# Kernel tuning notes

Measured on AMD Instinct MI355X. Metric: run time of the kernel, lower is better.

The kernel has to match this reference:

```python
import jax, jax.numpy as jnp
import numpy as np

D_HID = 512
N_HEADS = 16
D_HEAD = D_HID // N_HEADS  # 32
D_FFN = 2048
B, N = 4, 1024
FACTOR = 0.5 / np.sqrt(D_HEAD)
EPS = 1e-5


def layer_norm(x, g, b):
    m = x.mean(-1, keepdims=True)
    v = ((x - m) ** 2).mean(-1, keepdims=True)
    return (x - m) / jnp.sqrt(v + EPS) * g + b


def setup_inputs() -> dict:
    key = jax.random.key(0)
    ks = jax.random.split(key, 24)
    s = 0.02
    p = lambda k, shape: jax.random.normal(k, shape, jnp.float32) * s
    inp = {
        'H': jax.random.normal(ks[0], (B, N, D_HID), jnp.float32),
        'V': jax.random.normal(ks[1], (B, N, 3, D_HID), jnp.float32),
        'D_batch': jax.random.normal(ks[2], (B, N, N), jnp.float32),
        'rbf_bias': jax.random.normal(ks[3], (B, 1, N, N), jnp.float32),
        'H_mask': jax.random.randint(ks[4], (B, N), 0, 2, jnp.int32),
        # attention sublayer params
        'g1': jnp.ones((D_HID,), jnp.float32), 'beta1': jnp.zeros((D_HID,), jnp.float32),
        'Wq': p(ks[5], (D_HID, 4 * D_HID)), 'bq': p(ks[6], (4 * D_HID,)),
        'Wk': p(ks[7], (D_HID, 4 * D_HID)), 'bk': p(ks[8], (4 * D_HID,)),
        'Wv': p(ks[9], (D_HID, D_HID)), 'bv': p(ks[10], (D_HID,)),
        'Wvv': p(ks[11], (D_HID, D_HID)),
        'Wo': p(ks[12], (D_HID, D_HID)), 'bo': p(ks[13], (D_HID,)),
        'Wvo': p(ks[14], (D_HID, D_HID)),
        # GVP FFN sublayer params
        'g2': jnp.ones((D_HID,), jnp.float32), 'beta2': jnp.zeros((D_HID,), jnp.float32),
        'Wlv': p(ks[15], (D_HID, 2 * D_HID)),
        'W1': p(ks[16], (2 * D_HID, D_FFN)), 'b1f': p(ks[17], (D_FFN,)),
        'W2': p(ks[18], (D_FFN, 2 * D_HID)), 'b2f': p(ks[19], (2 * D_HID,)),
    }
    return inp


def ept_forward(H, V, D_batch, rbf_bias, H_mask, g1, beta1, Wq, bq, Wk, bk, Wv, bv,
                Wvv, Wo, bo, Wvo, g2, beta2, Wlv, W1, b1f, W2, b2f):
    b, n, d = H.shape
    # ---- attention sublayer (pre-LN on H only, residual on H and V) ----
    Hn = layer_norm(H, g1, beta1)
    Hq = (Hn @ Wq + bq).reshape(b, n, N_HEADS, 4 * D_HEAD)
    Hk = (Hn @ Wk + bk).reshape(b, n, N_HEADS, 4 * D_HEAD)
    Hv = (Hn @ Wv + bv).reshape(b, n, N_HEADS, D_HEAD)
    # vector values: [b,n,3,d] -> [b,n,heads,3*dh]
    Vv = (V @ Wvv).reshape(b, n, 3, N_HEADS, D_HEAD).transpose(0, 1, 3, 2, 4)
    Vv = Vv.reshape(b, n, N_HEADS, 3 * D_HEAD)
    V_attn = jnp.concatenate([Hv, Vv], axis=-1)  # [b,n,h,4*dh]
    bias = rbf_bias + D_batch[:, None]  # [b,1,n,n]
    keep = (H_mask != 0)[:, None, None, :]  # mask keys
    bias = jnp.where(keep, bias, -jnp.inf)
    logits = jnp.einsum('bnhd,bmhd->bhnm', Hq, Hk) * FACTOR + bias
    attn = jax.nn.softmax(logits, axis=-1)
    res = jnp.einsum('bhnm,bmhd->bnhd', attn, V_attn)  # [b,n,h,4*dh]
    H_res = res[..., :D_HEAD].reshape(b, n, d)
    V_res = res[..., D_HEAD:].reshape(b, n, N_HEADS, 3, D_HEAD)
    V_res = V_res.transpose(0, 1, 3, 2, 4).reshape(b, n, 3, d)
    H = H + H_res @ Wo + bo
    V = V + V_res @ Wvo
    # ---- GVP FFN sublayer (pre-LN on H only, residual) ----
    Hn2 = layer_norm(H, g2, beta2)
    Vp = V @ Wlv  # [b,n,3,2d]
    V1, V2 = Vp[..., :d], Vp[..., d:]
    scaler = jnp.concatenate([Hn2, jnp.sqrt((V1 ** 2).sum(axis=-2))], axis=-1)
    h = jax.nn.silu(scaler @ W1 + b1f) @ W2 + b2f  # [b,n,2d]
    H = H + h[..., :d]
    V = V + h[..., None, d:] * V2
    return H, V


def reference(H, V, D_batch, rbf_bias, H_mask, g1, beta1, Wq, bq, Wk, bk, Wv, bv,
              Wvv, Wo, bo, Wvo, g2, beta2, Wlv, W1, b1f, W2, b2f):
    return ept_forward(H, V, D_batch, rbf_bias, H_mask, g1, beta1, Wq, bq, Wk, bk,
                       Wv, bv, Wvv, Wo, bo, Wvo, g2, beta2, Wlv, W1, b1f, W2, b2f)
```

## Files before the change

kernel.cpp:

```cpp
#include <hip/hip_runtime.h>
#include <math.h>

#define NBATCH 4
#define NSEQ   1024
#define DHID   512
#define NHEADS 16
#define ROWS   (NBATCH*NSEQ)
#define VROWS  (ROWS*3)
#define ATT_FACTOR 0.08838834764831845f
#define LOG2E 1.4426950408889634f
#define F2 (ATT_FACTOR*LOG2E)
#define SM_SHIFT (16.0f*LOG2E)

typedef __attribute__((ext_vector_type(8))) short short8;
typedef __attribute__((ext_vector_type(4))) float floatx4;

#define AS1 __attribute__((address_space(1)))
#define AS3 __attribute__((address_space(3)))
#define GLOAD_LDS16(g, l) \
  __builtin_amdgcn_global_load_lds((const AS1 void*)(g), (AS3 void*)(l), 16, 0, 0)

__device__ __forceinline__ ushort f2bf(float x) {
  union { float f; unsigned u; } v; v.f = x;
  unsigned r = v.u + 0x7fff + ((v.u >> 16) & 1);
  return (ushort)(r >> 16);
}
__device__ __forceinline__ float bf2f(ushort u) {
  union { unsigned u; float f; } v; v.u = ((unsigned)u) << 16; return v.f;
}

template<int OBF>
__global__ __launch_bounds__(256) void ln_kernel(
    const float* __restrict__ x, void* __restrict__ y, int ystride,
    const float* __restrict__ g, const float* __restrict__ beta)
{
  int row = blockIdx.x;
  int t = threadIdx.x;
  const float* xr = x + (size_t)row * DHID;
  float2 v = ((const float2*)xr)[t];
  float s  = v.x + v.y;
  float ss = v.x*v.x + v.y*v.y;
  #pragma unroll
  for (int off = 32; off > 0; off >>= 1) {
    s  += __shfl_down(s, off);
    ss += __shfl_down(ss, off);
  }
  __shared__ float red[8];
  int w = t >> 6;
  if ((t & 63) == 0) { red[w*2] = s; red[w*2+1] = ss; }
  __syncthreads();
  s  = red[0] + red[2] + red[4] + red[6];
  ss = red[1] + red[3] + red[5] + red[7];
  float mean = s * (1.0f/DHID);
  float var  = ss * (1.0f/DHID) - mean*mean;
  float rstd = rsqrtf(var + 1e-5f);
  float2 gg = ((const float2*)g)[t];
  float2 bb = ((const float2*)beta)[t];
  float2 o;
  o.x = (v.x - mean) * rstd * gg.x + bb.x;
  o.y = (v.y - mean) * rstd * gg.y + bb.y;
  if constexpr (OBF) {
    ushort2 u = { f2bf(o.x), f2bf(o.y) };
    *(ushort2*)&((ushort*)y)[(size_t)row * ystride + 2*t] = u;
  } else {
    *(float2*)&((float*)y)[(size_t)row * ystride + 2*t] = o;
  }
}

struct WJobs {
  const float* src[9];
  ushort*      dst[9];
  int K[9];
  int N[9];
  int blk0[10];
};

__global__ __launch_bounds__(256) void wtrans_all_kernel(WJobs J)
{
  __shared__ float Ts[64][65];
  int bid = blockIdx.x;
  int j = 0;
  #pragma unroll
  for (int i = 1; i < 9; i++) if (bid >= J.blk0[i]) j = i;
  const float* W = J.src[j];
  ushort* Wt = J.dst[j];
  int K = J.K[j], N = J.N[j];
  int local = bid - J.blk0[j];
  int nx = N >> 6;
  int bx = local - (local / nx) * nx;
  int by = local / nx;
  int k0 = by*64, n0 = bx*64;
  int t = threadIdx.x;
  #pragma unroll
  for (int p = 0; p < 4; p++) {
    int f = p*256 + t;
    int r = f >> 4, c = (f & 15)*4;
    float4 v = *(const float4*)&W[(size_t)(k0+r)*N + n0 + c];
    Ts[r][c] = v.x; Ts[r][c+1] = v.y; Ts[r][c+2] = v.z; Ts[r][c+3] = v.w;
  }
  __syncthreads();
  #pragma unroll
  for (int p = 0; p < 2; p++) {
    int gidx = p*256 + t;
    int nr = gidx >> 3, kc = (gidx & 7)*8;
    ushort u[8];
    #pragma unroll
    for (int x = 0; x < 8; x++) u[x] = f2bf(Ts[kc+x][nr]);
    ushort4 a = {u[0],u[1],u[2],u[3]}, b4 = {u[4],u[5],u[6],u[7]};
    *(ushort4*)&Wt[(size_t)(n0+nr)*K + k0 + kc]     = a;
    *(ushort4*)&Wt[(size_t)(n0+nr)*K + k0 + kc + 4] = b4;
  }
}

__global__ __launch_bounds__(256) void conv_bf16_kernel(
    const float* __restrict__ x, ushort* __restrict__ y)
{
  int i = blockIdx.x*256 + threadIdx.x;
  float4 v = ((const float4*)x)[i];
  ushort4 u = { f2bf(v.x), f2bf(v.y), f2bf(v.z), f2bf(v.w) };
  ((ushort4*)y)[i] = u;
}

__global__ __launch_bounds__(256) void biascat_kernel(
    const float* __restrict__ bq, const float* __restrict__ bk,
    const float* __restrict__ bv, float* __restrict__ o)
{
  int i = blockIdx.x*256 + threadIdx.x;
  float v = (i < 2048) ? bq[i] : (i < 4096 ? bk[i-2048] : bv[i-4096]);
  o[i] = v;
}

template<int ACT, int HAS_BIAS, int HAS_RES, int OUT_BF16, int DUAL>
__global__ __launch_bounds__(256) void gemm_mfma_kernel(
    const ushort* __restrict__ A, const ushort* __restrict__ Bt,
    const float* __restrict__ bias, const float* __restrict__ resid,
    void* __restrict__ Cv, ushort* __restrict__ C2,
    int M, int N, int K)
{
  __shared__ ushort As[2][128*32];
  __shared__ ushort Bs[2][128*32];
  int t = threadIdx.x;
  int w = t >> 6, lane = t & 63;
  int q16 = lane & 15, quad = lane >> 4;
  int m0 = blockIdx.y * 128, n0 = blockIdx.x * 128;
  int wm = (w & 1) * 64, wn = (w >> 1) * 64;

  int r0 = t >> 2;
  int c0 = (t & 3) * 8;
  const ushort* Ag = A  + (size_t)(m0 + r0) * K + c0;
  const ushort* Bg = Bt + (size_t)(n0 + r0) * K + c0;
  int wb = w * 512;

  floatx4 acc[4][4];
  #pragma unroll
  for (int i = 0; i < 4; i++)
    #pragma unroll
    for (int j = 0; j < 4; j++) acc[i][j] = (floatx4){0.f,0.f,0.f,0.f};

  #define STAGE(buf, kk) do { \
    GLOAD_LDS16(Ag + (kk),                 &As[buf][wb]); \
    GLOAD_LDS16(Ag + (size_t)64*K + (kk),  &As[buf][2048 + wb]); \
    GLOAD_LDS16(Bg + (kk),                 &Bs[buf][wb]); \
    GLOAD_LDS16(Bg + (size_t)64*K + (kk),  &Bs[buf][2048 + wb]); \
  } while (0)

  STAGE(0, 0);
  __syncthreads();

  int nt = K >> 5;
  int cur = 0;
  for (int kt = 0; kt < nt; kt++) {
    if (kt + 1 < nt) STAGE(cur ^ 1, (kt + 1) * 32);
    short8 af[4], bf4[4];
    #pragma unroll
    for (int i = 0; i < 4; i++) {
      af[i]  = *(const short8*)&As[cur][(wm + i*16 + q16)*32 + quad*8];
      bf4[i] = *(const short8*)&Bs[cur][(wn + i*16 + q16)*32 + quad*8];
    }
    #pragma unroll
    for (int i = 0; i < 4; i++)
      #pragma unroll
      for (int j = 0; j < 4; j++)
        acc[i][j] = __builtin_amdgcn_mfma_f32_16x16x32_bf16(af[i], bf4[j], acc[i][j], 0, 0, 0);
    __syncthreads();
    cur ^= 1;
  }
  #undef STAGE

  float* Cf = (float*)Cv;
  ushort* Cu = (ushort*)Cv;
  float bj[4];
  #pragma unroll
  for (int j = 0; j < 4; j++)
    bj[j] = HAS_BIAS ? bias[n0 + wn + j*16 + q16] : 0.f;
  #pragma unroll
  for (int i = 0; i < 4; i++) {
    #pragma unroll
    for (int r = 0; r < 4; r++) {
      int row = m0 + wm + i*16 + quad*4 + r;
      size_t base = (size_t)row * N;
      #pragma unroll
      for (int j = 0; j < 4; j++) {
        int col = n0 + wn + j*16 + q16;
        float v = acc[i][j][r] + bj[j];
        if constexpr (ACT == 1) v = v / (1.f + __expf(-v));
        if constexpr (HAS_RES) v += resid[base + col];
        if constexpr (OUT_BF16) Cu[base + col] = f2bf(v);
        else                    Cf[base + col] = v;
        if constexpr (DUAL) C2[base + col] = f2bf(v);
      }
    }
  }
}

__global__ __launch_bounds__(256) void gemm_wovo_kernel(
    const ushort* __restrict__ A,
    const ushort* __restrict__ WoTp, const ushort* __restrict__ WvoTp,
    const float* __restrict__ bo,
    const float* __restrict__ Hres, const float* __restrict__ Vres,
    float* __restrict__ Hout, float* __restrict__ Vout,
    ushort* __restrict__ Voutbf)
{
  const int K = 512;
  __shared__ ushort As[2][128*32];
  __shared__ ushort Bs[2][128*32];
  int t = threadIdx.x;
  int w = t >> 6, lane = t & 63;
  int q16 = lane & 15, quad = lane >> 4;
  int m0 = blockIdx.y * 128, n0 = blockIdx.x * 128;
  int wm = (w & 1) * 64, wn = (w >> 1) * 64;
  bool inH = (m0 < 4096);
  const ushort* Bt = inH ? WoTp : WvoTp;

  int r0 = t >> 2;
  int c0 = (t & 3) * 8;
  const ushort* Ag = A  + (size_t)(m0 + r0) * K + c0;
  const ushort* Bg = Bt + (size_t)(n0 + r0) * K + c0;
  int wb = w * 512;

  floatx4 acc[4][4];
  #pragma unroll
  for (int i = 0; i < 4; i++)
    #pragma unroll
    for (int j = 0; j < 4; j++) acc[i][j] = (floatx4){0.f,0.f,0.f,0.f};

  #define STAGE(buf, kk) do { \
    GLOAD_LDS16(Ag + (kk),                 &As[buf][wb]); \
    GLOAD_LDS16(Ag + (size_t)64*K + (kk),  &As[buf][2048 + wb]); \
    GLOAD_LDS16(Bg + (kk),                 &Bs[buf][wb]); \
    GLOAD_LDS16(Bg + (size_t)64*K + (kk),  &Bs[buf][2048 + wb]); \
  } while (0)

  STAGE(0, 0);
  __syncthreads();

  int cur = 0;
  for (int kt = 0; kt < 16; kt++) {
    if (kt + 1 < 16) STAGE(cur ^ 1, (kt + 1) * 32);
    short8 af[4], bf4[4];
    #pragma unroll
    for (int i = 0; i < 4; i++) {
      af[i]  = *(const short8*)&As[cur][(wm + i*16 + q16)*32 + quad*8];
      bf4[i] = *(const short8*)&Bs[cur][(wn + i*16 + q16)*32 + quad*8];
    }
    #pragma unroll
    for (int i = 0; i < 4; i++)
      #pragma unroll
      for (int j = 0; j < 4; j++)
        acc[i][j] = __builtin_amdgcn_mfma_f32_16x16x32_bf16(af[i], bf4[j], acc[i][j], 0, 0, 0);
    __syncthreads();
    cur ^= 1;
  }
  #undef STAGE

  float bj[4];
  #pragma unroll
  for (int j = 0; j < 4; j++)
    bj[j] = inH ? bo[n0 + wn + j*16 + q16] : 0.f;
  #pragma unroll
  for (int i = 0; i < 4; i++) {
    #pragma unroll
    for (int r = 0; r < 4; r++) {
      int row = m0 + wm + i*16 + quad*4 + r;
      #pragma unroll
      for (int j = 0; j < 4; j++) {
        int col = n0 + wn + j*16 + q16;
        float v = acc[i][j][r] + bj[j];
        if (inH) {
          size_t idx = (size_t)row * 512 + col;
          Hout[idx] = v + Hres[idx];
        } else {
          size_t idx = (size_t)(row - 4096) * 512 + col;
          float vv = v + Vres[idx];
          Vout[idx] = vv;
          Voutbf[idx] = f2bf(vv);
        }
      }
    }
  }
}

__global__ __launch_bounds__(256) void gemm_w2_finale_kernel(
    const ushort* __restrict__ A, const ushort* __restrict__ Bt,
    const float* __restrict__ bias, const float* __restrict__ VP,
    float* __restrict__ Hout, float* __restrict__ Vout)
{
  const int K = 2048;
  __shared__ ushort As[2][128*32];
  __shared__ ushort Bs[2][128*32];
  int t = threadIdx.x;
  int w = t >> 6, lane = t & 63;
  int q16 = lane & 15, quad = lane >> 4;
  int m0 = blockIdx.y * 128, n0 = blockIdx.x * 128;
  int wm = (w & 1) * 64, wn = (w >> 1) * 64;

  int r0 = t >> 2;
  int c0 = (t & 3) * 8;
  const ushort* Ag = A  + (size_t)(m0 + r0) * K + c0;
  const ushort* Bg = Bt + (size_t)(n0 + r0) * K + c0;
  int wb = w * 512;

  floatx4 acc[4][4];
  #pragma unroll
  for (int i = 0; i < 4; i++)
    #pragma unroll
    for (int j = 0; j < 4; j++) acc[i][j] = (floatx4){0.f,0.f,0.f,0.f};

  #define STAGE(buf, kk) do { \
    GLOAD_LDS16(Ag + (kk),                 &As[buf][wb]); \
    GLOAD_LDS16(Ag + (size_t)64*K + (kk),  &As[buf][2048 + wb]); \
    GLOAD_LDS16(Bg + (kk),                 &Bs[buf][wb]); \
    GLOAD_LDS16(Bg + (size_t)64*K + (kk),  &Bs[buf][2048 + wb]); \
  } while (0)

  STAGE(0, 0);
  __syncthreads();

  int cur = 0;
  for (int kt = 0; kt < 64; kt++) {
    if (kt + 1 < 64) STAGE(cur ^ 1, (kt + 1) * 32);
    short8 af[4], bf4[4];
    #pragma unroll
    for (int i = 0; i < 4; i++) {
      af[i]  = *(const short8*)&As[cur][(wm + i*16 + q16)*32 + quad*8];
      bf4[i] = *(const short8*)&Bs[cur][(wn + i*16 + q16)*32 + quad*8];
    }
    #pragma unroll
    for (int i = 0; i < 4; i++)
      #pragma unroll
      for (int j = 0; j < 4; j++)
        acc[i][j] = __builtin_amdgcn_mfma_f32_16x16x32_bf16(af[i], bf4[j], acc[i][j], 0, 0, 0);
    __syncthreads();
    cur ^= 1;
  }
  #undef STAGE

  float bj[4];
  #pragma unroll
  for (int j = 0; j < 4; j++)
    bj[j] = bias[n0 + wn + j*16 + q16];
  bool inH = (n0 < 512);
  #pragma unroll
  for (int i = 0; i < 4; i++) {
    #pragma unroll
    for (int r = 0; r < 4; r++) {
      int row = m0 + wm + i*16 + quad*4 + r;
      #pragma unroll
      for (int j = 0; j < 4; j++) {
        int col = n0 + wn + j*16 + q16;
        float v = acc[i][j][r] + bj[j];
        if (inH) {
          Hout[(size_t)row * 512 + col] += v;
        } else {
          int d = col - 512;
          #pragma unroll
          for (int c = 0; c < 3; c++) {
            size_t r3 = (size_t)(row * 3 + c);
            Vout[r3 * 512 + d] += v * VP[r3 * 1024 + 512 + d];
          }
        }
      }
    }
  }
}

__global__ __launch_bounds__(256) void bias2_kernel(
    const float* __restrict__ Db, const float* __restrict__ Rb,
    const int* __restrict__ Mask, ushort* __restrict__ Bc2)
{
  int i2 = blockIdx.x*256 + threadIdx.x;
  int e = i2 * 2;
  int b = e >> 20;
  int m = e & 1023;
  float2 d = *(const float2*)&Db[e];
  float2 r = *(const float2*)&Rb[e];
  ushort2 o;
  o.x = Mask[b*NSEQ + m]     ? f2bf((d.x + r.x)*LOG2E) : f2bf(-1e30f);
  o.y = Mask[b*NSEQ + m + 1] ? f2bf((d.y + r.y)*LOG2E) : f2bf(-1e30f);
  *(ushort2*)&Bc2[e] = o;
}

__global__ __launch_bounds__(256) void vtrans_kernel(
    const ushort* __restrict__ QKV, const ushort* __restrict__ VVr,
    ushort* __restrict__ Vt)
{
  __shared__ float Ts[64][33];
  int t = threadIdx.x;
  int bh = blockIdx.z;
  int b = bh >> 4, h = bh & 15;
  int dt = blockIdx.y;
  int nt = blockIdx.x;
  int d0 = dt*32, n0 = nt*64;
  #pragma unroll
  for (int i = 0; i < 2; i++) {
    int nl = (t >> 3) + i*32;
    int c4 = (t & 7)*4;
    const ushort* src;
    if (dt == 0) src = &QKV[(size_t)(b*NSEQ + n0 + nl)*4608 + 4096 + h*32 + c4];
    else { int c = dt - 1; src = &VVr[((size_t)(b*NSEQ + n0 + nl)*3 + c)*512 + h*32 + c4]; }
    ushort4 v = *(const ushort4*)src;
    Ts[nl][c4] = bf2f(v.x); Ts[nl][c4+1] = bf2f(v.y);
    Ts[nl][c4+2] = bf2f(v.z); Ts[nl][c4+3] = bf2f(v.w);
  }
  __syncthreads();
  int dl = t >> 3;
  int n8 = (t & 7)*8;
  ushort u[8];
  #pragma unroll
  for (int k = 0; k < 8; k++) u[k] = f2bf(Ts[n8+k][dl]);
  size_t ob = ((size_t)bh*128 + d0 + dl)*NSEQ + n0 + n8;
  ushort4 u0 = {u[0],u[1],u[2],u[3]}, u1 = {u[4],u[5],u[6],u[7]};
  *(ushort4*)&Vt[ob]     = u0;
  *(ushort4*)&Vt[ob + 4] = u1;
}

__global__ __launch_bounds__(256, 2) void attn_mfma_kernel(
    const ushort* __restrict__ QKV,
    const ushort* __restrict__ Vt, const ushort* __restrict__ Bc2,
    ushort* __restrict__ HRES, ushort* __restrict__ VRES)
{
  __shared__ union {
    ushort q[128][136];
    struct {
      ushort k[64][136];
      ushort v[128][72];
      ushort bias[128][72];
    } s;
  } S;
  __shared__ ushort Ps[4][32][72];

  int t = threadIdx.x;
  int w = t >> 6, lane = t & 63;
  int q16 = lane & 15, quad = lane >> 4;
  int h = blockIdx.x, qt = blockIdx.y, b = blockIdx.z;
  int q0 = qt * 128;

  float4 rk0, rk1, rk2, rk3;
  float4 rv0, rv1, rv2, rv3;
  float4 rb0, rb1, rb2, rb3;
  const size_t kbase = (size_t)(b*NSEQ)*4608 + 2048 + h*128 + (t&3)*8;
  const size_t vbase = ((size_t)(b*NHEADS + h)*128 + (t>>3))*NSEQ + (t&7)*8;
  const size_t bbase = (size_t)(b*NSEQ + q0 + (t>>3))*NSEQ + (t&7)*8;
  int kr = t >> 2;
  int kc = (t & 3)*8;
  int vr = t >> 3, vc = (t & 7)*8;

  #define LOADT(m0_) do { \
    const ushort* kp = &QKV[kbase + (size_t)((m0_) + kr)*4608]; \
    rk0 = *(const float4*)(kp +  0); \
    rk1 = *(const float4*)(kp + 32); \
    rk2 = *(const float4*)(kp + 64); \
    rk3 = *(const float4*)(kp + 96); \
    const ushort* vp = &Vt[vbase + (m0_)]; \
    rv0 = *(const float4*)(vp + (size_t) 0*NSEQ); \
    rv1 = *(const float4*)(vp + (size_t)32*NSEQ); \
    rv2 = *(const float4*)(vp + (size_t)64*NSEQ); \
    rv3 = *(const float4*)(vp + (size_t)96*NSEQ); \
    const ushort* bp2 = &Bc2[bbase + (m0_)]; \
    rb0 = *(const float4*)(bp2 + (size_t) 0*NSEQ); \
    rb1 = *(const float4*)(bp2 + (size_t)32*NSEQ); \
    rb2 = *(const float4*)(bp2 + (size_t)64*NSEQ); \
    rb3 = *(const float4*)(bp2 + (size_t)96*NSEQ); \
  } while (0)

  #define STORET() do { \
    *(float4*)&S.s.k[kr][kc +  0] = rk0; \
    *(float4*)&S.s.k[kr][kc + 32] = rk1; \
    *(float4*)&S.s.k[kr][kc + 64] = rk2; \
    *(float4*)&S.s.k[kr][kc + 96] = rk3; \
    *(float4*)&S.s.v[vr +  0][vc] = rv0; \
    *(float4*)&S.s.v[vr + 32][vc] = rv1; \
    *(float4*)&S.s.v[vr + 64][vc] = rv2; \
    *(float4*)&S.s.v[vr + 96][vc] = rv3; \
    *(float4*)&S.s.bias[vr +  0][vc] = rb0; \
    *(float4*)&S.s.bias[vr + 32][vc] = rb1; \
    *(float4*)&S.s.bias[vr + 64][vc] = rb2; \
    *(float4*)&S.s.bias[vr + 96][vc] = rb3; \
  } while (0)

  LOADT(0);

  #pragma unroll
  for (int i = 0; i < 8; i++) {
    int f = t + i*256;
    int r = f >> 4, c8 = f & 15;
    *(float4*)&S.q[r][c8*8] =
        *(const float4*)&QKV[(size_t)(b*NSEQ + q0 + r)*4608 + h*128 + c8*8];
  }
  __syncthreads();
  short8 qf[2][4];
  #pragma unroll
  for (int rg = 0; rg < 2; rg++)
    #pragma unroll
    for (int c = 0; c < 4; c++)
      qf[rg][c] = *(const short8*)&S.q[w*32 + rg*16 + q16][c*32 + quad*8];

  floatx4 o[2][8];
  #pragma unroll
  for (int rg = 0; rg < 2; rg++)
    #pragma unroll
    for (int i = 0; i < 8; i++) o[rg][i] = (floatx4){0.f,0.f,0.f,0.f};
  float l_i[2] = {0.f, 0.f};

  #pragma unroll 1
  for (int it = 0; it < 16; it++) {
    __syncthreads();
    STORET();
    if (it < 15) LOADT((it + 1) * 64);
    __syncthreads();

    floatx4 sf[2][4];
    #pragma unroll
    for (int rg = 0; rg < 2; rg++)
      #pragma unroll
      for (int g = 0; g < 4; g++) sf[rg][g] = (floatx4){0.f,0.f,0.f,0.f};
    __builtin_amdgcn_s_setprio(1);
    #pragma unroll
    for (int c = 0; c < 4; c++) {
      short8 kf[4];
      #pragma unroll
      for (int g = 0; g < 4; g++)
        kf[g] = *(const short8*)&S.s.k[g*16 + q16][c*32 + quad*8];
      #pragma unroll
      for (int rg = 0; rg < 2; rg++)
        #pragma unroll
        for (int g = 0; g < 4; g++)
          sf[rg][g] = __builtin_amdgcn_mfma_f32_16x16x32_bf16(kf[g], qf[rg][c], sf[rg][g], 0, 0, 0);
    }
    __builtin_amdgcn_s_setprio(0);

    #pragma unroll
    for (int rg = 0; rg < 2; rg++) {
      int brow = w*32 + rg*16 + q16;
      #pragma unroll
      for (int g = 0; g < 4; g++) {
        ushort4 bb = *(const ushort4*)&S.s.bias[brow][g*16 + quad*4];
        float p0 = exp2f(sf[rg][g][0]*F2 + bf2f(bb.x) - SM_SHIFT);
        float p1 = exp2f(sf[rg][g][1]*F2 + bf2f(bb.y) - SM_SHIFT);
        float p2 = exp2f(sf[rg][g][2]*F2 + bf2f(bb.z) - SM_SHIFT);
        float p3 = exp2f(sf[rg][g][3]*F2 + bf2f(bb.w) - SM_SHIFT);
        l_i[rg] += (p0 + p1) + (p2 + p3);
        unsigned d0, d1;
        asm("v_cvt_pk_bf16_f32 %0, %1, %2" : "=v"(d0) : "v"(p0), "v"(p1));
        asm("v_cvt_pk_bf16_f32 %0, %1, %2" : "=v"(d1) : "v"(p2), "v"(p3));
        uint2 dd = { d0, d1 };
        *(uint2*)&Ps[w][rg*16 + q16][g*16 + quad*4] = dd;
      }
    }

    short8 pf[2][2];
    #pragma unroll
    for (int rg = 0; rg < 2; rg++)
      #pragma unroll
      for (int ks = 0; ks < 2; ks++)
        pf[rg][ks] = *(const short8*)&Ps[w][rg*16 + q16][ks*32 + quad*8];
    __builtin_amdgcn_s_setprio(1);
    #pragma unroll
    for (int tt = 0; tt < 8; tt++) {
      short8 vf0 = *(const short8*)&S.s.v[tt*16 + q16][quad*8];
      short8 vf1 = *(const short8*)&S.s.v[tt*16 + q16][32 + quad*8];
      #pragma unroll
      for (int rg = 0; rg < 2; rg++) {
        o[rg][tt] = __builtin_amdgcn_mfma_f32_16x16x32_bf16(pf[rg][0], vf0, o[rg][tt], 0, 0, 0);
        o[rg][tt] = __builtin_amdgcn_mfma_f32_16x16x32_bf16(pf[rg][1], vf1, o[rg][tt], 0, 0, 0);
      }
    }
    __builtin_amdgcn_s_setprio(0);
  }
  #undef LOADT
  #undef STORET

  #pragma unroll
  for (int rg = 0; rg < 2; rg++) {
    float l = l_i[rg];
    l += __shfl_xor(l, 16);
    l += __shfl_xor(l, 32);
    #pragma unroll
    for (int i = 0; i < 4; i++) {
      float li = __shfl(l, quad*4 + i);
      float inv = 1.0f / li;
      int grow = b*NSEQ + q0 + w*32 + rg*16 + quad*4 + i;
      #pragma unroll
      for (int tt = 0; tt < 2; tt++)
        HRES[(size_t)grow*512 + h*32 + tt*16 + q16] = f2bf(o[rg][tt][i] * inv);
      #pragma unroll
      for (int tt = 2; tt < 8; tt++) {
        int c = (tt - 2) >> 1;
        int jj = ((tt - 2) & 1)*16 + q16;
        VRES[((size_t)grow*3 + c)*512 + h*32 + jj] = f2bf(o[rg][tt][i] * inv);
      }
    }
  }
}

__global__ __launch_bounds__(256) void vnorm_kernel(
    const float* __restrict__ VP, ushort* __restrict__ SC)
{
  int idx = blockIdx.x*256 + threadIdx.x;
  int row = idx >> 9;
  int d = idx & 511;
  const float* p = VP + (size_t)row*3072 + d;
  float a = p[0], b = p[1024], c = p[2048];
  SC[(size_t)row*1024 + 512 + d] = f2bf(sqrtf(a*a + b*b + c*c));
}

extern "C" void kernel_launch(void* const* d_in, const int* in_sizes, int n_in,
                              void* d_out, int out_size, void* d_ws, size_t ws_size,
                              hipStream_t stream)
{
  const float* H    = (const float*)d_in[0];
  const float* V    = (const float*)d_in[1];
  const float* Db   = (const float*)d_in[2];
  const float* Rb   = (const float*)d_in[3];
  const int*   Mask = (const int*)d_in[4];
  const float* g1   = (const float*)d_in[5];
  const float* be1  = (const float*)d_in[6];
  const float* Wq   = (const float*)d_in[7];
  const float* bq   = (const float*)d_in[8];
  const float* Wk   = (const float*)d_in[9];
  const float* bkk  = (const float*)d_in[10];
  const float* Wv   = (const float*)d_in[11];
  const float* bv   = (const float*)d_in[12];
  const float* Wvv  = (const float*)d_in[13];
  const float* Wo   = (const float*)d_in[14];
  const float* bo   = (const float*)d_in[15];
  const float* Wvo  = (const float*)d_in[16];
  const float* g2   = (const float*)d_in[17];
  const float* be2  = (const float*)d_in[18];
  const float* Wlv  = (const float*)d_in[19];
  const float* W1   = (const float*)d_in[20];
  const float* b1f  = (const float*)d_in[21];
  const float* W2   = (const float*)d_in[22];
  const float* b2f  = (const float*)d_in[23];

  float* Hout = (float*)d_out;
  float* Vout = Hout + (size_t)ROWS*DHID;

  char* w = (char*)d_ws;
  const size_t MB = 1024*1024;
  const size_t KB = 1024;
  ushort* WqT  = (ushort*)(w + 0);
  ushort* WkT  = (ushort*)(w + 2048*KB);
  ushort* WvT  = (ushort*)(w + 4096*KB);
  ushort* WvvT = (ushort*)(w + 4608*KB);
  ushort* WoT  = (ushort*)(w + 5120*KB);
  ushort* WvoT = (ushort*)(w + 5632*KB);
  ushort* WlvT = (ushort*)(w + 6144*KB);
  ushort* W1T  = (ushort*)(w + 7168*KB);
  ushort* W2T  = (ushort*)(w + 11264*KB);
  float*  Bqkv = (float*)(w + 15360*KB);
  ushort* HNbf  = (ushort*)(w + 16*MB);
  ushort* QKVbf = (ushort*)(w + 20*MB);
  ushort* VVrbf = (ushort*)(w + 56*MB);
  ushort* Vbf   = (ushort*)(w + 68*MB);
  ushort* Vtb   = (ushort*)(w + 80*MB);
  ushort* Bc2   = (ushort*)(w + 96*MB);
  ushort* HRESbf = (ushort*)(w + 104*MB);
  ushort* VRESbf = (ushort*)(w + 108*MB);
  ushort* Voutbf = (ushort*)(w + 20*MB);
  float*  VP     = (float*)(w + 56*MB);
  ushort* SCbf   = (ushort*)(w + 104*MB);
  ushort* S1bf   = (ushort*)(w + 112*MB);

  dim3 blk(256);

  WJobs J;
  const float* ws_[9] = {Wq, Wk, Wv, Wvv, Wo, Wvo, Wlv, W1, W2};
  ushort* wd_[9] = {WqT, WkT, WvT, WvvT, WoT, WvoT, WlvT, W1T, W2T};
  int wk_[9] = {512, 512, 512, 512, 512, 512, 512, 1024, 2048};
  int wn_[9] = {2048, 2048, 512, 512, 512, 512, 1024, 2048, 1024};
  int off = 0;
  for (int i = 0; i < 9; i++) {
    J.src[i] = ws_[i]; J.dst[i] = wd_[i]; J.K[i] = wk_[i]; J.N[i] = wn_[i];
    J.blk0[i] = off;
    off += (wn_[i] >> 6) * (wk_[i] >> 6);
  }
  J.blk0[9] = off;
  wtrans_all_kernel<<<off, blk, 0, stream>>>(J);

  ln_kernel<1><<<ROWS, blk, 0, stream>>>(H, HNbf, DHID, g1, be1);
  conv_bf16_kernel<<<(VROWS*DHID/4)/256, blk, 0, stream>>>(V, Vbf);
  biascat_kernel<<<18, blk, 0, stream>>>(bq, bkk, bv, Bqkv);

  gemm_mfma_kernel<0,1,0,1,0><<<dim3(36, 32), blk, 0, stream>>>(HNbf, WqT, Bqkv, nullptr, QKVbf, nullptr, 4096, 4608, 512);
  gemm_mfma_kernel<0,0,0,1,0><<<dim3( 4, 96), blk, 0, stream>>>(Vbf, WvvT, nullptr, nullptr, VVrbf, nullptr, 12288, 512, 512);

  bias2_kernel<<<(NBATCH*NSEQ*NSEQ/2)/256, blk, 0, stream>>>(Db, Rb, Mask, Bc2);
  vtrans_kernel<<<dim3(16, 4, 64), blk, 0, stream>>>(QKVbf, VVrbf, Vtb);

  attn_mfma_kernel<<<dim3(16, 8, 4), blk, 0, stream>>>(QKVbf, Vtb, Bc2, HRESbf, VRESbf);

  gemm_wovo_kernel<<<dim3(4, 128), blk, 0, stream>>>(HRESbf, WoT, WvoT, bo, H, V, Hout, Vout, Voutbf);

  ln_kernel<1><<<ROWS, blk, 0, stream>>>(Hout, SCbf, 1024, g2, be2);
  gemm_mfma_kernel<0,0,0,0,0><<<dim3(8, 96), blk, 0, stream>>>(Voutbf, WlvT, nullptr, nullptr, VP, nullptr, 12288, 1024, 512);
  vnorm_kernel<<<(ROWS*DHID)/256, blk, 0, stream>>>(VP, SCbf);

  gemm_mfma_kernel<1,1,0,1,0><<<dim3(16, 32), blk, 0, stream>>>(SCbf, W1T, b1f, nullptr, S1bf, nullptr, 4096, 2048, 1024);
  gemm_w2_finale_kernel<<<dim3(8, 32), blk, 0, stream>>>(S1bf, W2T, b2f, VP, Hout, Vout);
}
```

Measured before the change: 479.1 us.

## Split W2 GEMM from its residual epilogue and halve the M tile

The W2 GEMM no longer applies the H residual and the gated V update in its epilogue. It now writes a plain fp32 result to a workspace buffer, and a separate elementwise finale kernel applies both updates with coalesced accesses. The GEMM tile shrinks from 128x128 to 64x128, which doubles the grid to 512 blocks for better CU occupancy on a 4096x1024x2048 problem. The cost is one extra launch plus a 16MB write and read of the intermediate, in exchange for removing the scattered strided read-modify-writes in the epilogue.

```diff
diff --git a/kernel.cpp b/kernel.cpp
--- a/kernel.cpp
+++ b/kernel.cpp
@@ -300,19 +300,18 @@
   }
 }
 
-__global__ __launch_bounds__(256) void gemm_w2_finale_kernel(
+__global__ __launch_bounds__(256) void gemm_w2_kernel(
     const ushort* __restrict__ A, const ushort* __restrict__ Bt,
-    const float* __restrict__ bias, const float* __restrict__ VP,
-    float* __restrict__ Hout, float* __restrict__ Vout)
-{
-  const int K = 2048;
-  __shared__ ushort As[2][128*32];
+    const float* __restrict__ bias, float* __restrict__ C)
+{
+  const int N = 1024, K = 2048;
+  __shared__ ushort As[2][64*32];
   __shared__ ushort Bs[2][128*32];
   int t = threadIdx.x;
   int w = t >> 6, lane = t & 63;
   int q16 = lane & 15, quad = lane >> 4;
-  int m0 = blockIdx.y * 128, n0 = blockIdx.x * 128;
-  int wm = (w & 1) * 64, wn = (w >> 1) * 64;
+  int m0 = blockIdx.y * 64, n0 = blockIdx.x * 128;
+  int wm = (w & 1) * 32, wn = (w >> 1) * 64;
 
   int r0 = t >> 2;
   int c0 = (t & 3) * 8;
@@ -320,15 +319,14 @@
   const ushort* Bg = Bt + (size_t)(n0 + r0) * K + c0;
   int wb = w * 512;
 
-  floatx4 acc[4][4];
-  #pragma unroll
-  for (int i = 0; i < 4; i++)
+  floatx4 acc[2][4];
+  #pragma unroll
+  for (int i = 0; i < 2; i++)
     #pragma unroll
     for (int j = 0; j < 4; j++) acc[i][j] = (floatx4){0.f,0.f,0.f,0.f};
 
   #define STAGE(buf, kk) do { \
     GLOAD_LDS16(Ag + (kk),                 &As[buf][wb]); \
-    GLOAD_LDS16(Ag + (size_t)64*K + (kk),  &As[buf][2048 + wb]); \
     GLOAD_LDS16(Bg + (kk),                 &Bs[buf][wb]); \
     GLOAD_LDS16(Bg + (size_t)64*K + (kk),  &Bs[buf][2048 + wb]); \
   } while (0)
@@ -339,14 +337,15 @@
   int cur = 0;
   for (int kt = 0; kt < 64; kt++) {
     if (kt + 1 < 64) STAGE(cur ^ 1, (kt + 1) * 32);
-    short8 af[4], bf4[4];
-    #pragma unroll
-    for (int i = 0; i < 4; i++) {
+    short8 af[2], bf4[4];
+    #pragma unroll
+    for (int i = 0; i < 2; i++)
       af[i]  = *(const short8*)&As[cur][(wm + i*16 + q16)*32 + quad*8];
-      bf4[i] = *(const short8*)&Bs[cur][(wn + i*16 + q16)*32 + quad*8];
-    }
-    #pragma unroll
-    for (int i = 0; i < 4; i++)
+    #pragma unroll
+    for (int j = 0; j < 4; j++)
+      bf4[j] = *(const short8*)&Bs[cur][(wn + j*16 + q16)*32 + quad*8];
+    #pragma unroll
+    for (int i = 0; i < 2; i++)
       #pragma unroll
       for (int j = 0; j < 4; j++)
         acc[i][j] = __builtin_amdgcn_mfma_f32_16x16x32_bf16(af[i], bf4[j], acc[i][j], 0, 0, 0);
@@ -359,26 +358,15 @@
   #pragma unroll
   for (int j = 0; j < 4; j++)
     bj[j] = bias[n0 + wn + j*16 + q16];
-  bool inH = (n0 < 512);
-  #pragma unroll
-  for (int i = 0; i < 4; i++) {
+  #pragma unroll
+  for (int i = 0; i < 2; i++) {
     #pragma unroll
     for (int r = 0; r < 4; r++) {
       int row = m0 + wm + i*16 + quad*4 + r;
       #pragma unroll
       for (int j = 0; j < 4; j++) {
         int col = n0 + wn + j*16 + q16;
-        float v = acc[i][j][r] + bj[j];
-        if (inH) {
-          Hout[(size_t)row * 512 + col] += v;
-        } else {
-          int d = col - 512;
-          #pragma unroll
-          for (int c = 0; c < 3; c++) {
-            size_t r3 = (size_t)(row * 3 + c);
-            Vout[r3 * 512 + d] += v * VP[r3 * 1024 + 512 + d];
-          }
-        }
+        C[(size_t)row * N + col] = acc[i][j][r] + bj[j];
       }
     }
   }
@@ -622,6 +610,24 @@
   const float* p = VP + (size_t)row*3072 + d;
   float a = p[0], b = p[1024], c = p[2048];
   SC[(size_t)row*1024 + 512 + d] = f2bf(sqrtf(a*a + b*b + c*c));
+}
+
+__global__ __launch_bounds__(256) void finale_kernel(
+    const float* __restrict__ HH, const float* __restrict__ VP,
+    float* __restrict__ Hout, float* __restrict__ Vout)
+{
+  int idx = blockIdx.x*256 + threadIdx.x;
+  if (idx < ROWS*DHID) {
+    int row = idx >> 9;
+    int d = idx & 511;
+    Hout[idx] += HH[(size_t)row*1024 + d];
+  } else {
+    int k = idx - ROWS*DHID;
+    int r3 = k >> 9;
+    int d = k & 511;
+    int row = r3 / 3;
+    Vout[k] += HH[(size_t)row*1024 + 512 + d] * VP[(size_t)r3*1024 + 512 + d];
+  }
 }
 
 extern "C" void kernel_launch(void* const* d_in, const int* in_sizes, int n_in,
@@ -681,6 +687,7 @@
   float*  VP     = (float*)(w + 56*MB);
   ushort* SCbf   = (ushort*)(w + 104*MB);
   ushort* S1bf   = (ushort*)(w + 112*MB);
+  float*  HHb    = (float*)(w + 32*MB);
 
   dim3 blk(256);
 
@@ -717,5 +724,6 @@
   vnorm_kernel<<<(ROWS*DHID)/256, blk, 0, stream>>>(VP, SCbf);
 
   gemm_mfma_kernel<1,1,0,1,0><<<dim3(16, 32), blk, 0, stream>>>(SCbf, W1T, b1f, nullptr, S1bf, nullptr, 4096, 2048, 1024);
-  gemm_w2_finale_kernel<<<dim3(8, 32), blk, 0, stream>>>(S1bf, W2T, b2f, VP, Hout, Vout);
-}
+  gemm_w2_kernel<<<dim3(8, 64), blk, 0, stream>>>(S1bf, W2T, b2f, HHb);
+  finale_kernel<<<((ROWS + VROWS)*DHID)/256, blk, 0, stream>>>(HHb, VP, Hout, Vout);
+}
```

New measurement: 468.0 us. 2.3% less time.
